# Performance work log

Measured on AMD Instinct MI355X. Metric: run time of the kernel, lower is better.

## Reference

```python
import jax, jax.numpy as jnp
import numpy as np

B, N, DIM = 2, 2048, 256
HEADS, DHEAD = 8, 32
INNER = HEADS * DHEAD


def setup_inputs() -> dict:
    key = jax.random.key(0)
    ks = jax.random.split(key, 8)
    w = 0.05  # weight scale for numerical stability
    return {
        "x_r": jax.random.normal(ks[0], (B, N, DIM), jnp.float32),
        "x_i": jax.random.normal(ks[1], (B, N, DIM), jnp.float32),
        "Wq_r": jax.random.normal(ks[2], (INNER, DIM), jnp.float32) * w,
        "Wq_i": jax.random.normal(ks[3], (INNER, DIM), jnp.float32) * w,
        "Wkv_r": jax.random.normal(ks[4], (2 * INNER, DIM), jnp.float32) * w,
        "Wkv_i": jax.random.normal(ks[5], (2 * INNER, DIM), jnp.float32) * w,
        "Wo_r": jax.random.normal(ks[6], (DIM, INNER), jnp.float32) * w,
        "Wo_i": jax.random.normal(ks[7], (DIM, INNER), jnp.float32) * w,
    }


def _clinear(xr, xi, Wr, Wi):
    # complex linear y = x @ W^T with W as nn.Linear weight (out, in)
    yr = xr @ Wr.T - xi @ Wi.T
    yi = xr @ Wi.T + xi @ Wr.T
    return yr, yi


def _split_heads(t):  # b n (h d) -> b h n d
    b, n, hd = t.shape
    return t.reshape(b, n, HEADS, DHEAD).transpose(0, 2, 1, 3)


def reference(x_r, x_i, Wq_r, Wq_i, Wkv_r, Wkv_i, Wo_r, Wo_i):
    qr, qi = _clinear(x_r, x_i, Wq_r, Wq_i)
    kvr, kvi = _clinear(x_r, x_i, Wkv_r, Wkv_i)
    kr, vr = jnp.split(kvr, 2, axis=-1)
    ki, vi = jnp.split(kvi, 2, axis=-1)
    qr, qi, kr, ki, vr, vi = map(_split_heads, (qr, qi, kr, ki, vr, vi))

    # complete complex attention: 4 real attention passes stacked on axis r
    q_s = jnp.stack([qr, qr, qi, qi], axis=0)      # r b h n d
    k_s = jnp.stack([kr, -ki, kr, -ki], axis=0)
    v_s = jnp.stack([vr, vr, vi, vi], axis=0)

    scale = DHEAD ** -0.5
    scores = jnp.einsum('rbhnd,rbhmd->rbhnm', q_s, k_s) * scale
    attn = jax.nn.softmax(scores, axis=-1)
    out = jnp.einsum('rbhnm,rbhmd->rbhnd', attn, v_s)

    rr, ri, ir, ii = out[0], out[1], out[2], out[3]
    o_r = rr - ii
    o_i = ri + ir

    # merge heads: b h n d -> b n (h d)
    o_r = o_r.transpose(0, 2, 1, 3).reshape(B, N, INNER)
    o_i = o_i.transpose(0, 2, 1, 3).reshape(B, N, INNER)

    y_r, y_i = _clinear(o_r, o_i, Wo_r, Wo_i)
    return jnp.stack([y_r, y_i], axis=-1)  # (B, N, DIM, 2) = complex as real/imag
```

## Files before the change

kernel.cpp:

```cpp
#include <hip/hip_runtime.h>

#define SC_LOG2 0.25503486f

typedef __bf16 bf16x8 __attribute__((ext_vector_type(8)));
typedef __bf16 bf16x2 __attribute__((ext_vector_type(2)));
typedef float f32x4 __attribute__((ext_vector_type(4)));
typedef unsigned int u32x4 __attribute__((ext_vector_type(4)));

union FragU { u32x4 u; bf16x8 b; };

__device__ __forceinline__ unsigned short f2bf(float f) {
  return __builtin_bit_cast(unsigned short, (__bf16)f);
}
__device__ __forceinline__ unsigned int pkbf(float a, float b) {
  bf16x2 v = { (__bf16)a, (__bf16)b };
  return __builtin_bit_cast(unsigned int, v);
}

__device__ __forceinline__ void glds16(const void* g, void* l) {
  __builtin_amdgcn_global_load_lds(
      (const __attribute__((address_space(1))) unsigned int*)g,
      (__attribute__((address_space(3))) unsigned int*)l, 16, 0, 0);
}

__global__ __launch_bounds__(256) void prep_x(const float* __restrict__ xr,
                                              const float* __restrict__ xi,
                                              unsigned short* __restrict__ Xbf) {
  int idx = blockIdx.x * 256 + threadIdx.x;
  int m = idx >> 6;
  int c8 = (idx & 63) << 3;
  const float* src = (c8 < 256) ? (xr + (size_t)m * 256 + c8)
                                : (xi + (size_t)m * 256 + (c8 - 256));
  float4 a = *(const float4*)src;
  float4 b = *(const float4*)(src + 4);
  u32x4 o;
  o.x = pkbf(a.x, a.y);
  o.y = pkbf(a.z, a.w);
  o.z = pkbf(b.x, b.y);
  o.w = pkbf(b.z, b.w);
  *(u32x4*)(Xbf + (size_t)m * 512 + c8) = o;
}

__global__ __launch_bounds__(256) void prep_w(const float* __restrict__ Wq_r,
                                              const float* __restrict__ Wq_i,
                                              const float* __restrict__ Wkv_r,
                                              const float* __restrict__ Wkv_i,
                                              const float* __restrict__ Wo_r,
                                              const float* __restrict__ Wo_i,
                                              unsigned short* __restrict__ Wc1,
                                              unsigned short* __restrict__ Wc2) {
  int idx = blockIdx.x * 256 + threadIdx.x;
  int row = idx >> 6;
  int c8 = (idx & 63) << 3;
  bool hi = (c8 >= 256);
  int cc = hi ? (c8 - 256) : c8;
  const float* lo_p; const float* hi_p; float hsgn;
  unsigned short* dst;
  if (row < 1536) {
    int sec = row >> 8, o = row & 255;
    switch (sec) {
      case 0:  lo_p = Wq_r + (size_t)o * 256;          hi_p = Wq_i + (size_t)o * 256;          hsgn = -1.f; break;
      case 1:  lo_p = Wq_i + (size_t)o * 256;          hi_p = Wq_r + (size_t)o * 256;          hsgn =  1.f; break;
      case 2:  lo_p = Wkv_r + (size_t)o * 256;         hi_p = Wkv_i + (size_t)o * 256;         hsgn = -1.f; break;
      case 3:  lo_p = Wkv_i + (size_t)o * 256;         hi_p = Wkv_r + (size_t)o * 256;         hsgn =  1.f; break;
      case 4:  lo_p = Wkv_r + (size_t)(256 + o) * 256; hi_p = Wkv_i + (size_t)(256 + o) * 256; hsgn = -1.f; break;
      default: lo_p = Wkv_i + (size_t)(256 + o) * 256; hi_p = Wkv_r + (size_t)(256 + o) * 256; hsgn =  1.f; break;
    }
    dst = Wc1 + (size_t)row * 512 + c8;
  } else {
    int r2 = row - 1536; int comp = r2 & 1; int o = r2 >> 1;
    lo_p = comp ? (Wo_i + (size_t)o * 256) : (Wo_r + (size_t)o * 256);
    hi_p = comp ? (Wo_r + (size_t)o * 256) : (Wo_i + (size_t)o * 256);
    hsgn = comp ? 1.f : -1.f;
    dst = Wc2 + (size_t)r2 * 512 + c8;
  }
  const float* src = hi ? hi_p : lo_p;
  float sgn = hi ? hsgn : 1.f;
  if (row < 512) sgn *= SC_LOG2;
  float4 a = *(const float4*)(src + cc);
  float4 b = *(const float4*)(src + cc + 4);
  u32x4 o4;
  o4.x = pkbf(a.x * sgn, a.y * sgn);
  o4.y = pkbf(a.z * sgn, a.w * sgn);
  o4.z = pkbf(b.x * sgn, b.y * sgn);
  o4.w = pkbf(b.z * sgn, b.w * sgn);
  *(u32x4*)dst = o4;
}

template<int NT>
__device__ __forceinline__ void gemm_core(const unsigned short* __restrict__ A,
                                          const unsigned short* __restrict__ W,
                                          int m0, int o0, unsigned short* lds,
                                          f32x4 (&acc)[4][NT / 32]) {
  int t = threadIdx.x;
  int lane = t & 63, w = t >> 6;
  int l15 = lane & 15, g = lane >> 4;
  int wm = w >> 1, wn = w & 1;
  unsigned short* ldsB = lds + 4096;
  const unsigned short* ga = A + (size_t)(m0 + (t & 127)) * 512 + (t >> 7) * 8;
  const unsigned short* gw = (NT == 128)
      ? W + (size_t)(o0 + (t & 127)) * 512 + (t >> 7) * 8
      : W + (size_t)(o0 + (t & 63)) * 512 + (t >> 6) * 8;
  for (int kt = 0; kt < 16; ++kt) {
    glds16(ga + kt * 32, lds + t * 8);
    glds16(ga + 16 + kt * 32, lds + 2048 + t * 8);
    if constexpr (NT == 128) {
      glds16(gw + kt * 32, ldsB + t * 8);
      glds16(gw + 16 + kt * 32, ldsB + 2048 + t * 8);
    } else {
      glds16(gw + kt * 32, ldsB + t * 8);
    }
    __syncthreads();
    FragU a[4], b[NT / 32];
#pragma unroll
    for (int sm = 0; sm < 4; ++sm)
      a[sm].u = *(const u32x4*)(lds + g * 1024 + (wm * 64 + sm * 16 + l15) * 8);
#pragma unroll
    for (int sn = 0; sn < NT / 32; ++sn) {
      if constexpr (NT == 128)
        b[sn].u = *(const u32x4*)(ldsB + g * 1024 + (wn * 64 + sn * 16 + l15) * 8);
      else
        b[sn].u = *(const u32x4*)(ldsB + g * 512 + (wn * 32 + sn * 16 + l15) * 8);
    }
#pragma unroll
    for (int sm = 0; sm < 4; ++sm)
#pragma unroll
      for (int sn = 0; sn < NT / 32; ++sn)
        acc[sm][sn] = __builtin_amdgcn_mfma_f32_16x16x32_bf16(a[sm].b, b[sn].b, acc[sm][sn], 0, 0, 0);
    __syncthreads();
  }
}

__global__ __launch_bounds__(256) void gemm_qkv(const unsigned short* __restrict__ Xbf,
                                                const unsigned short* __restrict__ Wc1,
                                                unsigned short* __restrict__ Qr,
                                                unsigned short* __restrict__ Qi,
                                                unsigned short* __restrict__ Kr,
                                                unsigned short* __restrict__ Ki,
                                                unsigned short* __restrict__ Vrt,
                                                unsigned short* __restrict__ Vit) {
  __shared__ __align__(16) unsigned short lds[8448];
  int bid = blockIdx.x;
  int m0 = (bid / 12) * 128, o0 = (bid % 12) * 128;
  f32x4 acc[4][4];
#pragma unroll
  for (int i = 0; i < 4; ++i)
#pragma unroll
    for (int j = 0; j < 4; ++j) acc[i][j] = f32x4{0.f, 0.f, 0.f, 0.f};
  gemm_core<128>(Xbf, Wc1, m0, o0, lds, acc);
  int t = threadIdx.x;
  int lane = t & 63, w = t >> 6;
  int l15 = lane & 15, g = lane >> 4;
  int wm = w >> 1, wn = w & 1;
  if (o0 >= 1024) {
#pragma unroll
    for (int h = 0; h < 2; ++h) {
      if (wn == h) {
#pragma unroll
        for (int sn = 0; sn < 4; ++sn) {
          int ol = sn * 16 + l15;
#pragma unroll
          for (int sm = 0; sm < 4; ++sm)
#pragma unroll
            for (int r = 0; r < 4; ++r)
              lds[ol * 132 + wm * 64 + sm * 16 + 4 * g + r] = f2bf(acc[sm][sn][r]);
        }
      }
      __syncthreads();
      {
        int ol = t >> 2, mc = (t & 3) * 32;
        int o = o0 + h * 64 + ol;
        int oo = o & 255, dd = oo & 31, hh = oo >> 5;
        int bh = (m0 >> 11) * 8 + hh;
        int n = (m0 & 2047) + mc;
        unsigned short* dstp = ((o >> 8) == 4 ? Vrt : Vit) + ((size_t)bh * 32 + dd) * 2048 + n;
#pragma unroll
        for (int q = 0; q < 4; ++q)
          *(u32x4*)(dstp + q * 8) = *(const u32x4*)(lds + ol * 132 + mc + q * 8);
      }
      if (h == 0) __syncthreads();
    }
  } else {
#pragma unroll
    for (int sn = 0; sn < 4; ++sn) {
      int o = o0 + wn * 64 + sn * 16 + l15;
      int sec = o >> 8;
      int oo = o & 255;
      int hh = oo >> 5, dd = oo & 31;
#pragma unroll
      for (int sm = 0; sm < 4; ++sm)
#pragma unroll
        for (int r = 0; r < 4; ++r) {
          int m = m0 + wm * 64 + sm * 16 + 4 * g + r;
          int b = m >> 11, n = m & 2047;
          int bh = b * 8 + hh;
          unsigned short v = f2bf(acc[sm][sn][r]);
          switch (sec) {
            case 0:  Qr[((size_t)bh * 2048 + n) * 32 + dd] = v; break;
            case 1:  Qi[((size_t)bh * 2048 + n) * 32 + dd] = v; break;
            case 2:  Kr[((size_t)bh * 2048 + n) * 32 + dd] = v; break;
            default: Ki[((size_t)bh * 2048 + n) * 32 + dd] = v; break;
          }
        }
    }
  }
}

__global__ __launch_bounds__(256) void gemm_out(const unsigned short* __restrict__ Obf,
                                                const unsigned short* __restrict__ Wc2,
                                                float* __restrict__ out) {
  __shared__ __align__(16) unsigned short lds[6144];
  int m0 = (blockIdx.x >> 3) * 128, o0 = (blockIdx.x & 7) * 64;
  f32x4 acc[4][2];
#pragma unroll
  for (int i = 0; i < 4; ++i)
#pragma unroll
    for (int j = 0; j < 2; ++j) acc[i][j] = f32x4{0.f, 0.f, 0.f, 0.f};
  gemm_core<64>(Obf, Wc2, m0, o0, lds, acc);
  int lane = threadIdx.x & 63, w = threadIdx.x >> 6;
  int l15 = lane & 15, g = lane >> 4;
  int wm = w >> 1, wn = w & 1;
#pragma unroll
  for (int sm = 0; sm < 4; ++sm)
#pragma unroll
    for (int sn = 0; sn < 2; ++sn) {
      int o = o0 + wn * 32 + sn * 16 + l15;
#pragma unroll
      for (int r = 0; r < 4; ++r) {
        int m = m0 + wm * 64 + sm * 16 + 4 * g + r;
        out[(size_t)m * 512 + o] = acc[sm][sn][r];
      }
    }
}

__global__ __launch_bounds__(256) void attn(const unsigned short* __restrict__ Qr,
                                            const unsigned short* __restrict__ Qi,
                                            const unsigned short* __restrict__ Kr,
                                            const unsigned short* __restrict__ Ki,
                                            const unsigned short* __restrict__ Vrt,
                                            const unsigned short* __restrict__ Vit,
                                            unsigned short* __restrict__ Obf) {
  __shared__ __align__(16) char smem[49152];
  unsigned short* kv = (unsigned short*)smem;

  int bid = blockIdx.x;
  int bh = bid >> 6;
  int q0 = (bid & 63) * 32;
  int t = threadIdx.x;
  int p = t >> 6, lane = t & 63;
  int l15 = lane & 15, g = lane >> 4;

  const unsigned short* Qsel = (p & 2) ? Qi : Qr;
  FragU qf[2];
#pragma unroll
  for (int s = 0; s < 2; ++s)
    qf[s].u = *(const u32x4*)(Qsel + ((size_t)bh * 2048 + q0 + s * 16 + l15) * 32 + g * 8);
  if (p & 1) {
#pragma unroll
    for (int s = 0; s < 2; ++s) qf[s].u ^= 0x80008000u;
  }

  f32x4 acc[2][2];
#pragma unroll
  for (int s = 0; s < 2; ++s) { acc[s][0] = f32x4{0.f,0.f,0.f,0.f}; acc[s][1] = f32x4{0.f,0.f,0.f,0.f}; }
  float l_acc[2] = {0.f, 0.f};

  int i7 = t & 127;
  int passk = (t < 128) ? 0 : 1;
  const unsigned short* Ksrc = passk ? Ki : Kr;
  const unsigned short* Vsrc = passk ? Vit : Vrt;
  size_t kb0 = ((size_t)bh * 2048 + (i7 & 63)) * 32 + (i7 >> 6) * 8;
  size_t vb0 = ((size_t)bh * 32 + (i7 & 31)) * 2048 + (i7 >> 5) * 8;
  unsigned short* Pw = kv + 16384 + p * 2048;

  auto stage = [&](int ck, int nb) {
    int n0 = ck * 64;
    unsigned short* kd = kv + nb * 4096 + passk * 2048 + i7 * 8;
    unsigned short* vd = kv + 8192 + nb * 4096 + passk * 2048 + i7 * 8;
    glds16(Ksrc + kb0 + (size_t)n0 * 32, kd);
    glds16(Ksrc + kb0 + 16 + (size_t)n0 * 32, kd + 1024);
    glds16(Vsrc + vb0 + n0, vd);
    glds16(Vsrc + vb0 + 32 + n0, vd + 1024);
  };

  stage(0, 0);
  __syncthreads();

  for (int ck = 0; ck < 32; ++ck) {
    int cur = ck & 1;
    if (ck + 1 < 32) stage(ck + 1, cur ^ 1);
    const unsigned short* Ktile = kv + cur * 4096 + ((p & 1) ? 2048 : 0);
    const unsigned short* Vtile = kv + 8192 + cur * 4096 + ((p & 2) ? 2048 : 0);

    f32x4 st[4][2];
    __builtin_amdgcn_s_setprio(1);
#pragma unroll
    for (int c = 0; c < 4; ++c) {
      FragU kf; kf.u = *(const u32x4*)(Ktile + g * 512 + (c * 16 + l15) * 8);
#pragma unroll
      for (int s = 0; s < 2; ++s)
        st[c][s] = __builtin_amdgcn_mfma_f32_16x16x32_bf16(kf.b, qf[s].b, f32x4{0.f,0.f,0.f,0.f}, 0, 0, 0);
    }
    __builtin_amdgcn_s_setprio(0);

#pragma unroll
    for (int s = 0; s < 2; ++s) {
#pragma unroll
      for (int c = 0; c < 4; ++c) {
        float p0 = __builtin_amdgcn_exp2f(st[c][s][0]);
        float p1 = __builtin_amdgcn_exp2f(st[c][s][1]);
        float p2 = __builtin_amdgcn_exp2f(st[c][s][2]);
        float p3 = __builtin_amdgcn_exp2f(st[c][s][3]);
        l_acc[s] += (p0 + p1) + (p2 + p3);
        unsigned int w0 = pkbf(p0, p1);
        unsigned int w1 = pkbf(p2, p3);
        int eo = (c >> 1) * 1024 + (2 * (c & 1) + (g >> 1)) * 256 + (s * 16 + l15) * 8 + 4 * (g & 1);
        unsigned long long pv = (unsigned long long)w0 | ((unsigned long long)w1 << 32);
        *(unsigned long long*)(Pw + eo) = pv;
      }
    }

    __builtin_amdgcn_s_setprio(1);
#pragma unroll
    for (int kh = 0; kh < 2; ++kh) {
      FragU vf0, vf1;
      vf0.u = *(const u32x4*)(Vtile + (4 * kh + g) * 256 + l15 * 8);
      vf1.u = *(const u32x4*)(Vtile + (4 * kh + g) * 256 + (16 + l15) * 8);
#pragma unroll
      for (int s = 0; s < 2; ++s) {
        FragU pf; pf.u = *(const u32x4*)(Pw + kh * 1024 + g * 256 + (s * 16 + l15) * 8);
        acc[s][0] = __builtin_amdgcn_mfma_f32_16x16x32_bf16(pf.b, vf0.b, acc[s][0], 0, 0, 0);
        acc[s][1] = __builtin_amdgcn_mfma_f32_16x16x32_bf16(pf.b, vf1.b, acc[s][1], 0, 0, 0);
      }
    }
    __builtin_amdgcn_s_setprio(0);
    __syncthreads();
  }

  float linv[2];
#pragma unroll
  for (int s = 0; s < 2; ++s) {
    float lt = l_acc[s];
    lt += __shfl_xor(lt, 16);
    lt += __shfl_xor(lt, 32);
    linv[s] = 1.0f / lt;
  }
  float* ox = (float*)smem;
  if (p >= 2) {
    float* base = ox + ((p == 3) ? 0 : 1056);
#pragma unroll
    for (int s = 0; s < 2; ++s)
#pragma unroll
      for (int h = 0; h < 2; ++h)
#pragma unroll
        for (int r = 0; r < 4; ++r)
          base[(s * 16 + 4 * g + r) * 33 + 16 * h + l15] = acc[s][h][r] * __shfl(linv[s], 4 * g + r);
  }
  __syncthreads();
  if (p < 2) {
    const float* base = ox + ((p == 0) ? 0 : 1056);
    int coloff = (p == 0) ? 0 : 256;
    int b = bh >> 3, hh = bh & 7;
#pragma unroll
    for (int s = 0; s < 2; ++s)
#pragma unroll
      for (int h = 0; h < 2; ++h)
#pragma unroll
        for (int r = 0; r < 4; ++r) {
          float own = acc[s][h][r] * __shfl(linv[s], 4 * g + r);
          float part = base[(s * 16 + 4 * g + r) * 33 + 16 * h + l15];
          float res = (p == 0) ? (own - part) : (own + part);
          int q = q0 + s * 16 + 4 * g + r;
          Obf[((size_t)b * 2048 + q) * 512 + coloff + hh * 32 + 16 * h + l15] = f2bf(res);
        }
  }
}

extern "C" void kernel_launch(void* const* d_in, const int* in_sizes, int n_in,
                              void* d_out, int out_size, void* d_ws, size_t ws_size,
                              hipStream_t stream) {
  const float* xr    = (const float*)d_in[0];
  const float* xi    = (const float*)d_in[1];
  const float* Wq_r  = (const float*)d_in[2];
  const float* Wq_i  = (const float*)d_in[3];
  const float* Wkv_r = (const float*)d_in[4];
  const float* Wkv_i = (const float*)d_in[5];
  const float* Wo_r  = (const float*)d_in[6];
  const float* Wo_i  = (const float*)d_in[7];
  char* ws = (char*)d_ws;
  unsigned short* Xbf = (unsigned short*)(ws);
  unsigned short* Wc1 = (unsigned short*)(ws + 4194304);
  unsigned short* Wc2 = (unsigned short*)(ws + 5767168);
  unsigned short* Qr  = (unsigned short*)(ws + 6291456);
  unsigned short* Qi  = (unsigned short*)(ws + 8388608);
  unsigned short* Kr  = (unsigned short*)(ws + 10485760);
  unsigned short* Ki  = (unsigned short*)(ws + 12582912);
  unsigned short* Vrt = (unsigned short*)(ws + 14680064);
  unsigned short* Vit = (unsigned short*)(ws + 16777216);
  unsigned short* Obf = (unsigned short*)(ws + 18874368);
  float* out = (float*)d_out;

  prep_x<<<dim3(1024), dim3(256), 0, stream>>>(xr, xi, Xbf);
  prep_w<<<dim3(512), dim3(256), 0, stream>>>(Wq_r, Wq_i, Wkv_r, Wkv_i, Wo_r, Wo_i, Wc1, Wc2);
  gemm_qkv<<<dim3(384), dim3(256), 0, stream>>>(Xbf, Wc1, Qr, Qi, Kr, Ki, Vrt, Vit);
  attn<<<dim3(1024), dim3(256), 0, stream>>>(Qr, Qi, Kr, Ki, Vrt, Vit, Obf);
  gemm_out<<<dim3(256), dim3(256), 0, stream>>>(Obf, Wc2, out);
}
```

Measured before the change: 182.1 us.

## Fuse fp32-to-bf16 conversion of inputs and weights into GEMM tile loads

Removes the separate prep_x and prep_w kernels. The QKV and output GEMMs now read fp32 activations and weights directly, convert them to bf16 with the sign and scale folded in, and write them to LDS. Register prefetch of the next k-tile overlaps the global loads with the MFMA work. This saves two launches and the bf16 staging round trip through global memory. In exchange the direct global-to-LDS async loads are replaced by register staging, fp32 reads are twice as wide, and weight conversion is repeated in every block.

```diff
diff --git a/kernel.cpp b/kernel.cpp
--- a/kernel.cpp
+++ b/kernel.cpp
@@ -8,6 +8,7 @@
 typedef unsigned int u32x4 __attribute__((ext_vector_type(4)));
 
 union FragU { u32x4 u; bf16x8 b; };
+struct F8 { float4 lo, hi; };
 
 __device__ __forceinline__ unsigned short f2bf(float f) {
   return __builtin_bit_cast(unsigned short, (__bf16)f);
@@ -15,6 +16,25 @@
 __device__ __forceinline__ unsigned int pkbf(float a, float b) {
   bf16x2 v = { (__bf16)a, (__bf16)b };
   return __builtin_bit_cast(unsigned int, v);
+}
+__device__ __forceinline__ F8 ldf8(const float* p) {
+  F8 r; r.lo = *(const float4*)p; r.hi = *(const float4*)(p + 4); return r;
+}
+__device__ __forceinline__ void cv8s(unsigned short* d, const F8& v, float s) {
+  u32x4 o;
+  o.x = pkbf(v.lo.x * s, v.lo.y * s);
+  o.y = pkbf(v.lo.z * s, v.lo.w * s);
+  o.z = pkbf(v.hi.x * s, v.hi.y * s);
+  o.w = pkbf(v.hi.z * s, v.hi.w * s);
+  *(u32x4*)d = o;
+}
+__device__ __forceinline__ void cv8n(unsigned short* d, const F8& v) {
+  u32x4 o;
+  o.x = pkbf(v.lo.x, v.lo.y);
+  o.y = pkbf(v.lo.z, v.lo.w);
+  o.z = pkbf(v.hi.x, v.hi.y);
+  o.w = pkbf(v.hi.z, v.hi.w);
+  *(u32x4*)d = o;
 }
 
 __device__ __forceinline__ void glds16(const void* g, void* l) {
@@ -23,116 +43,12 @@
       (__attribute__((address_space(3))) unsigned int*)l, 16, 0, 0);
 }
 
-__global__ __launch_bounds__(256) void prep_x(const float* __restrict__ xr,
-                                              const float* __restrict__ xi,
-                                              unsigned short* __restrict__ Xbf) {
-  int idx = blockIdx.x * 256 + threadIdx.x;
-  int m = idx >> 6;
-  int c8 = (idx & 63) << 3;
-  const float* src = (c8 < 256) ? (xr + (size_t)m * 256 + c8)
-                                : (xi + (size_t)m * 256 + (c8 - 256));
-  float4 a = *(const float4*)src;
-  float4 b = *(const float4*)(src + 4);
-  u32x4 o;
-  o.x = pkbf(a.x, a.y);
-  o.y = pkbf(a.z, a.w);
-  o.z = pkbf(b.x, b.y);
-  o.w = pkbf(b.z, b.w);
-  *(u32x4*)(Xbf + (size_t)m * 512 + c8) = o;
-}
-
-__global__ __launch_bounds__(256) void prep_w(const float* __restrict__ Wq_r,
-                                              const float* __restrict__ Wq_i,
-                                              const float* __restrict__ Wkv_r,
-                                              const float* __restrict__ Wkv_i,
-                                              const float* __restrict__ Wo_r,
-                                              const float* __restrict__ Wo_i,
-                                              unsigned short* __restrict__ Wc1,
-                                              unsigned short* __restrict__ Wc2) {
-  int idx = blockIdx.x * 256 + threadIdx.x;
-  int row = idx >> 6;
-  int c8 = (idx & 63) << 3;
-  bool hi = (c8 >= 256);
-  int cc = hi ? (c8 - 256) : c8;
-  const float* lo_p; const float* hi_p; float hsgn;
-  unsigned short* dst;
-  if (row < 1536) {
-    int sec = row >> 8, o = row & 255;
-    switch (sec) {
-      case 0:  lo_p = Wq_r + (size_t)o * 256;          hi_p = Wq_i + (size_t)o * 256;          hsgn = -1.f; break;
-      case 1:  lo_p = Wq_i + (size_t)o * 256;          hi_p = Wq_r + (size_t)o * 256;          hsgn =  1.f; break;
-      case 2:  lo_p = Wkv_r + (size_t)o * 256;         hi_p = Wkv_i + (size_t)o * 256;         hsgn = -1.f; break;
-      case 3:  lo_p = Wkv_i + (size_t)o * 256;         hi_p = Wkv_r + (size_t)o * 256;         hsgn =  1.f; break;
-      case 4:  lo_p = Wkv_r + (size_t)(256 + o) * 256; hi_p = Wkv_i + (size_t)(256 + o) * 256; hsgn = -1.f; break;
-      default: lo_p = Wkv_i + (size_t)(256 + o) * 256; hi_p = Wkv_r + (size_t)(256 + o) * 256; hsgn =  1.f; break;
-    }
-    dst = Wc1 + (size_t)row * 512 + c8;
-  } else {
-    int r2 = row - 1536; int comp = r2 & 1; int o = r2 >> 1;
-    lo_p = comp ? (Wo_i + (size_t)o * 256) : (Wo_r + (size_t)o * 256);
-    hi_p = comp ? (Wo_r + (size_t)o * 256) : (Wo_i + (size_t)o * 256);
-    hsgn = comp ? 1.f : -1.f;
-    dst = Wc2 + (size_t)r2 * 512 + c8;
-  }
-  const float* src = hi ? hi_p : lo_p;
-  float sgn = hi ? hsgn : 1.f;
-  if (row < 512) sgn *= SC_LOG2;
-  float4 a = *(const float4*)(src + cc);
-  float4 b = *(const float4*)(src + cc + 4);
-  u32x4 o4;
-  o4.x = pkbf(a.x * sgn, a.y * sgn);
-  o4.y = pkbf(a.z * sgn, a.w * sgn);
-  o4.z = pkbf(b.x * sgn, b.y * sgn);
-  o4.w = pkbf(b.z * sgn, b.w * sgn);
-  *(u32x4*)dst = o4;
-}
-
-template<int NT>
-__device__ __forceinline__ void gemm_core(const unsigned short* __restrict__ A,
-                                          const unsigned short* __restrict__ W,
-                                          int m0, int o0, unsigned short* lds,
-                                          f32x4 (&acc)[4][NT / 32]) {
-  int t = threadIdx.x;
-  int lane = t & 63, w = t >> 6;
-  int l15 = lane & 15, g = lane >> 4;
-  int wm = w >> 1, wn = w & 1;
-  unsigned short* ldsB = lds + 4096;
-  const unsigned short* ga = A + (size_t)(m0 + (t & 127)) * 512 + (t >> 7) * 8;
-  const unsigned short* gw = (NT == 128)
-      ? W + (size_t)(o0 + (t & 127)) * 512 + (t >> 7) * 8
-      : W + (size_t)(o0 + (t & 63)) * 512 + (t >> 6) * 8;
-  for (int kt = 0; kt < 16; ++kt) {
-    glds16(ga + kt * 32, lds + t * 8);
-    glds16(ga + 16 + kt * 32, lds + 2048 + t * 8);
-    if constexpr (NT == 128) {
-      glds16(gw + kt * 32, ldsB + t * 8);
-      glds16(gw + 16 + kt * 32, ldsB + 2048 + t * 8);
-    } else {
-      glds16(gw + kt * 32, ldsB + t * 8);
-    }
-    __syncthreads();
-    FragU a[4], b[NT / 32];
-#pragma unroll
-    for (int sm = 0; sm < 4; ++sm)
-      a[sm].u = *(const u32x4*)(lds + g * 1024 + (wm * 64 + sm * 16 + l15) * 8);
-#pragma unroll
-    for (int sn = 0; sn < NT / 32; ++sn) {
-      if constexpr (NT == 128)
-        b[sn].u = *(const u32x4*)(ldsB + g * 1024 + (wn * 64 + sn * 16 + l15) * 8);
-      else
-        b[sn].u = *(const u32x4*)(ldsB + g * 512 + (wn * 32 + sn * 16 + l15) * 8);
-    }
-#pragma unroll
-    for (int sm = 0; sm < 4; ++sm)
-#pragma unroll
-      for (int sn = 0; sn < NT / 32; ++sn)
-        acc[sm][sn] = __builtin_amdgcn_mfma_f32_16x16x32_bf16(a[sm].b, b[sn].b, acc[sm][sn], 0, 0, 0);
-    __syncthreads();
-  }
-}
-
-__global__ __launch_bounds__(256) void gemm_qkv(const unsigned short* __restrict__ Xbf,
-                                                const unsigned short* __restrict__ Wc1,
+__global__ __launch_bounds__(256) void gemm_qkv(const float* __restrict__ xr,
+                                                const float* __restrict__ xi,
+                                                const float* __restrict__ Wq_r,
+                                                const float* __restrict__ Wq_i,
+                                                const float* __restrict__ Wkv_r,
+                                                const float* __restrict__ Wkv_i,
                                                 unsigned short* __restrict__ Qr,
                                                 unsigned short* __restrict__ Qi,
                                                 unsigned short* __restrict__ Kr,
@@ -140,18 +56,73 @@
                                                 unsigned short* __restrict__ Vrt,
                                                 unsigned short* __restrict__ Vit) {
   __shared__ __align__(16) unsigned short lds[8448];
+  unsigned short* ldsB = lds + 4096;
   int bid = blockIdx.x;
   int m0 = (bid / 12) * 128, o0 = (bid % 12) * 128;
-  f32x4 acc[4][4];
-#pragma unroll
-  for (int i = 0; i < 4; ++i)
-#pragma unroll
-    for (int j = 0; j < 4; ++j) acc[i][j] = f32x4{0.f, 0.f, 0.f, 0.f};
-  gemm_core<128>(Xbf, Wc1, m0, o0, lds, acc);
   int t = threadIdx.x;
   int lane = t & 63, w = t >> 6;
   int l15 = lane & 15, g = lane >> 4;
   int wm = w >> 1, wn = w & 1;
+
+  int cb = (t >> 7) * 8;
+  int arow = m0 + (t & 127);
+  const float* xa_lo = xr + (size_t)arow * 256 + cb;
+  const float* xa_hi = xi + (size_t)arow * 256 + cb;
+  int wrow = o0 + (t & 127);
+  int sec = wrow >> 8, o = wrow & 255;
+  const float *wlo, *whi; float hsgn;
+  switch (sec) {
+    case 0:  wlo = Wq_r + (size_t)o * 256;          whi = Wq_i + (size_t)o * 256;          hsgn = -1.f; break;
+    case 1:  wlo = Wq_i + (size_t)o * 256;          whi = Wq_r + (size_t)o * 256;          hsgn =  1.f; break;
+    case 2:  wlo = Wkv_r + (size_t)o * 256;         whi = Wkv_i + (size_t)o * 256;         hsgn = -1.f; break;
+    case 3:  wlo = Wkv_i + (size_t)o * 256;         whi = Wkv_r + (size_t)o * 256;         hsgn =  1.f; break;
+    case 4:  wlo = Wkv_r + (size_t)(256 + o) * 256; whi = Wkv_i + (size_t)(256 + o) * 256; hsgn = -1.f; break;
+    default: wlo = Wkv_i + (size_t)(256 + o) * 256; whi = Wkv_r + (size_t)(256 + o) * 256; hsgn =  1.f; break;
+  }
+  float qsc = (wrow < 512) ? SC_LOG2 : 1.f;
+  float slo = qsc, shi = hsgn * qsc;
+  wlo += cb; whi += cb;
+
+  f32x4 acc[4][4];
+#pragma unroll
+  for (int i = 0; i < 4; ++i)
+#pragma unroll
+    for (int j = 0; j < 4; ++j) acc[i][j] = f32x4{0.f, 0.f, 0.f, 0.f};
+
+  F8 ra0 = ldf8(xa_lo), ra1 = ldf8(xa_lo + 16);
+  F8 rw0 = ldf8(wlo),   rw1 = ldf8(wlo + 16);
+  float s_cur = slo;
+
+  for (int kt = 0; kt < 16; ++kt) {
+    cv8n(lds + t * 8, ra0);
+    cv8n(lds + 2048 + t * 8, ra1);
+    cv8s(ldsB + t * 8, rw0, s_cur);
+    cv8s(ldsB + 2048 + t * 8, rw1, s_cur);
+    if (kt < 15) {
+      int kn = kt + 1;
+      int cw = (kn & 7) * 32;
+      const float* as = (kn < 8 ? xa_lo : xa_hi) + cw;
+      const float* ws = (kn < 8 ? wlo : whi) + cw;
+      ra0 = ldf8(as); ra1 = ldf8(as + 16);
+      rw0 = ldf8(ws); rw1 = ldf8(ws + 16);
+      s_cur = (kn < 8) ? slo : shi;
+    }
+    __syncthreads();
+    FragU a[4], b[4];
+#pragma unroll
+    for (int sm = 0; sm < 4; ++sm)
+      a[sm].u = *(const u32x4*)(lds + g * 1024 + (wm * 64 + sm * 16 + l15) * 8);
+#pragma unroll
+    for (int sn = 0; sn < 4; ++sn)
+      b[sn].u = *(const u32x4*)(ldsB + g * 1024 + (wn * 64 + sn * 16 + l15) * 8);
+#pragma unroll
+    for (int sm = 0; sm < 4; ++sm)
+#pragma unroll
+      for (int sn = 0; sn < 4; ++sn)
+        acc[sm][sn] = __builtin_amdgcn_mfma_f32_16x16x32_bf16(a[sm].b, b[sn].b, acc[sm][sn], 0, 0, 0);
+    __syncthreads();
+  }
+
   if (o0 >= 1024) {
 #pragma unroll
     for (int h = 0; h < 2; ++h) {
@@ -169,11 +140,11 @@
       __syncthreads();
       {
         int ol = t >> 2, mc = (t & 3) * 32;
-        int o = o0 + h * 64 + ol;
-        int oo = o & 255, dd = oo & 31, hh = oo >> 5;
+        int oc = o0 + h * 64 + ol;
+        int oo = oc & 255, dd = oo & 31, hh = oo >> 5;
         int bh = (m0 >> 11) * 8 + hh;
         int n = (m0 & 2047) + mc;
-        unsigned short* dstp = ((o >> 8) == 4 ? Vrt : Vit) + ((size_t)bh * 32 + dd) * 2048 + n;
+        unsigned short* dstp = ((oc >> 8) == 4 ? Vrt : Vit) + ((size_t)bh * 32 + dd) * 2048 + n;
 #pragma unroll
         for (int q = 0; q < 4; ++q)
           *(u32x4*)(dstp + q * 8) = *(const u32x4*)(lds + ol * 132 + mc + q * 8);
@@ -183,9 +154,9 @@
   } else {
 #pragma unroll
     for (int sn = 0; sn < 4; ++sn) {
-      int o = o0 + wn * 64 + sn * 16 + l15;
-      int sec = o >> 8;
-      int oo = o & 255;
+      int oc = o0 + wn * 64 + sn * 16 + l15;
+      int se = oc >> 8;
+      int oo = oc & 255;
       int hh = oo >> 5, dd = oo & 31;
 #pragma unroll
       for (int sm = 0; sm < 4; ++sm)
@@ -195,7 +166,7 @@
           int b = m >> 11, n = m & 2047;
           int bh = b * 8 + hh;
           unsigned short v = f2bf(acc[sm][sn][r]);
-          switch (sec) {
+          switch (se) {
             case 0:  Qr[((size_t)bh * 2048 + n) * 32 + dd] = v; break;
             case 1:  Qi[((size_t)bh * 2048 + n) * 32 + dd] = v; break;
             case 2:  Kr[((size_t)bh * 2048 + n) * 32 + dd] = v; break;
@@ -207,28 +178,68 @@
 }
 
 __global__ __launch_bounds__(256) void gemm_out(const unsigned short* __restrict__ Obf,
-                                                const unsigned short* __restrict__ Wc2,
+                                                const float* __restrict__ Wo_r,
+                                                const float* __restrict__ Wo_i,
                                                 float* __restrict__ out) {
   __shared__ __align__(16) unsigned short lds[6144];
+  unsigned short* ldsB = lds + 4096;
+  int t = threadIdx.x;
   int m0 = (blockIdx.x >> 3) * 128, o0 = (blockIdx.x & 7) * 64;
-  f32x4 acc[4][2];
-#pragma unroll
-  for (int i = 0; i < 4; ++i)
-#pragma unroll
-    for (int j = 0; j < 2; ++j) acc[i][j] = f32x4{0.f, 0.f, 0.f, 0.f};
-  gemm_core<64>(Obf, Wc2, m0, o0, lds, acc);
-  int lane = threadIdx.x & 63, w = threadIdx.x >> 6;
+  int lane = t & 63, w = t >> 6;
   int l15 = lane & 15, g = lane >> 4;
   int wm = w >> 1, wn = w & 1;
+
+  const unsigned short* ga = Obf + (size_t)(m0 + (t & 127)) * 512 + (t >> 7) * 8;
+  int r2 = o0 + (t & 63);
+  int comp = r2 & 1, o = r2 >> 1;
+  const float* wlo = (comp ? Wo_i : Wo_r) + (size_t)o * 256 + (t >> 6) * 8;
+  const float* whi = (comp ? Wo_r : Wo_i) + (size_t)o * 256 + (t >> 6) * 8;
+  float shi = comp ? 1.f : -1.f;
+
+  f32x4 acc[4][2];
+#pragma unroll
+  for (int i = 0; i < 4; ++i)
+#pragma unroll
+    for (int j = 0; j < 2; ++j) acc[i][j] = f32x4{0.f, 0.f, 0.f, 0.f};
+
+  F8 rw = ldf8(wlo);
+  float s_cur = 1.f;
+
+  for (int kt = 0; kt < 16; ++kt) {
+    glds16(ga + kt * 32, lds + t * 8);
+    glds16(ga + 16 + kt * 32, lds + 2048 + t * 8);
+    cv8s(ldsB + t * 8, rw, s_cur);
+    if (kt < 15) {
+      int kn = kt + 1;
+      const float* ws = (kn < 8 ? wlo : whi) + (kn & 7) * 32;
+      rw = ldf8(ws);
+      s_cur = (kn < 8) ? 1.f : shi;
+    }
+    __syncthreads();
+    FragU a[4], b[2];
+#pragma unroll
+    for (int sm = 0; sm < 4; ++sm)
+      a[sm].u = *(const u32x4*)(lds + g * 1024 + (wm * 64 + sm * 16 + l15) * 8);
+#pragma unroll
+    for (int sn = 0; sn < 2; ++sn)
+      b[sn].u = *(const u32x4*)(ldsB + g * 512 + (wn * 32 + sn * 16 + l15) * 8);
+#pragma unroll
+    for (int sm = 0; sm < 4; ++sm)
+#pragma unroll
+      for (int sn = 0; sn < 2; ++sn)
+        acc[sm][sn] = __builtin_amdgcn_mfma_f32_16x16x32_bf16(a[sm].b, b[sn].b, acc[sm][sn], 0, 0, 0);
+    __syncthreads();
+  }
+
 #pragma unroll
   for (int sm = 0; sm < 4; ++sm)
 #pragma unroll
     for (int sn = 0; sn < 2; ++sn) {
-      int o = o0 + wn * 32 + sn * 16 + l15;
+      int oc = o0 + wn * 32 + sn * 16 + l15;
 #pragma unroll
       for (int r = 0; r < 4; ++r) {
         int m = m0 + wm * 64 + sm * 16 + 4 * g + r;
-        out[(size_t)m * 512 + o] = acc[sm][sn][r];
+        out[(size_t)m * 512 + oc] = acc[sm][sn][r];
       }
     }
 }
@@ -388,21 +399,17 @@
   const float* Wo_r  = (const float*)d_in[6];
   const float* Wo_i  = (const float*)d_in[7];
   char* ws = (char*)d_ws;
-  unsigned short* Xbf = (unsigned short*)(ws);
-  unsigned short* Wc1 = (unsigned short*)(ws + 4194304);
-  unsigned short* Wc2 = (unsigned short*)(ws + 5767168);
-  unsigned short* Qr  = (unsigned short*)(ws + 6291456);
-  unsigned short* Qi  = (unsigned short*)(ws + 8388608);
-  unsigned short* Kr  = (unsigned short*)(ws + 10485760);
-  unsigned short* Ki  = (unsigned short*)(ws + 12582912);
-  unsigned short* Vrt = (unsigned short*)(ws + 14680064);
-  unsigned short* Vit = (unsigned short*)(ws + 16777216);
-  unsigned short* Obf = (unsigned short*)(ws + 18874368);
+  unsigned short* Qr  = (unsigned short*)(ws);
+  unsigned short* Qi  = (unsigned short*)(ws + 2097152);
+  unsigned short* Kr  = (unsigned short*)(ws + 4194304);
+  unsigned short* Ki  = (unsigned short*)(ws + 6291456);
+  unsigned short* Vrt = (unsigned short*)(ws + 8388608);
+  unsigned short* Vit = (unsigned short*)(ws + 10485760);
+  unsigned short* Obf = (unsigned short*)(ws + 12582912);
   float* out = (float*)d_out;
 
-  prep_x<<<dim3(1024), dim3(256), 0, stream>>>(xr, xi, Xbf);
-  prep_w<<<dim3(512), dim3(256), 0, stream>>>(Wq_r, Wq_i, Wkv_r, Wkv_i, Wo_r, Wo_i, Wc1, Wc2);
-  gemm_qkv<<<dim3(384), dim3(256), 0, stream>>>(Xbf, Wc1, Qr, Qi, Kr, Ki, Vrt, Vit);
+  gemm_qkv<<<dim3(384), dim3(256), 0, stream>>>(xr, xi, Wq_r, Wq_i, Wkv_r, Wkv_i,
+                                                Qr, Qi, Kr, Ki, Vrt, Vit);
   attn<<<dim3(1024), dim3(256), 0, stream>>>(Qr, Qi, Kr, Ki, Vrt, Vit, Obf);
-  gemm_out<<<dim3(256), dim3(256), 0, stream>>>(Obf, Wc2, out);
-}
+  gemm_out<<<dim3(256), dim3(256), 0, stream>>>(Obf, Wo_r, Wo_i, out);
+}
```

Result: slower. 192.9 us (+5.9%).
